# Kernel optimization log

Hardware: AMD Instinct MI355X
Metric: run time of the kernel (lower is better)

## Reference

```python
import jax, jax.numpy as jnp
import numpy as np

N_HEAD = 12
N_EMBED = 768

def setup_inputs() -> dict:
    key = jax.random.key(0)
    ks = jax.random.split(key, 5)
    B, T, C = 8, 1024, N_EMBED
    s_in = 1.0 / np.sqrt(C)
    s3 = 1.0 / np.sqrt(3 * C)
    return {
        "x": jax.random.normal(ks[0], (B, T, C), dtype=jnp.float32),
        "W_qkv": jax.random.normal(ks[1], (C, 3 * C), dtype=jnp.float32) * s_in,
        "b_qkv": jnp.zeros((3 * C,), dtype=jnp.float32),
        "W_out": jax.random.normal(ks[2], (C, C), dtype=jnp.float32) * s_in,
        "b_out": jnp.zeros((C,), dtype=jnp.float32),
    }

def reference(x, W_qkv, b_qkv, W_out, b_out):
    B, T, C = x.shape
    H = N_HEAD
    d_k = C // H
    qkv = x @ W_qkv + b_qkv  # [B,T,3C]
    q, k, v = jnp.split(qkv, 3, axis=-1)
    # [B,H,T,d]
    q = q.reshape(B, T, H, d_k).transpose(0, 2, 1, 3)
    k = k.reshape(B, T, H, d_k).transpose(0, 2, 1, 3)
    v = v.reshape(B, T, H, d_k).transpose(0, 2, 1, 3)
    logits = jnp.einsum('bhqd,bhkd->bhqk', q, k) * (d_k ** -0.5)
    causal = jnp.tril(jnp.ones((T, T), dtype=bool))
    logits = jnp.where(causal, logits, -jnp.inf)
    scores = jax.nn.softmax(logits, axis=-1)
    out = jnp.einsum('bhqk,bhkd->bhqd', scores, v)
    out = out.transpose(0, 2, 1, 3).reshape(B, T, C)
    return out @ W_out + b_out
```

## Files before the change

### kernel.cpp

```cpp
#include <hip/hip_runtime.h>
#include <stdint.h>

#define B_ 8
#define T_ 1024
#define C_ 768
#define H_ 12
#define DK 64
#define BT (B_*T_)
#define NQKV (3*C_)

typedef unsigned short u16;
typedef __bf16 bf16x8 __attribute__((ext_vector_type(8)));
typedef __bf16 bf16x4 __attribute__((ext_vector_type(4)));
typedef float  f32x4  __attribute__((ext_vector_type(4)));

typedef const __attribute__((address_space(1))) void gvoid_t;
typedef __attribute__((address_space(3))) void lvoid_t;

#define SBARRIER()  asm volatile("s_barrier" ::: "memory")
#define SWAITCNT(s) asm volatile("s_waitcnt " s ::: "memory")

__device__ __forceinline__ void gl_lds16(const void* g, void* l) {
    __builtin_amdgcn_global_load_lds((gvoid_t*)g, (lvoid_t*)l, 16, 0, 0);
}

__device__ __forceinline__ u16 f2b(float f) {
    union { float f; unsigned int u; } v; v.f = f;
    unsigned int u = v.u;
    return (u16)((u + 0x7fffu + ((u >> 16) & 1u)) >> 16);
}

__device__ __forceinline__ f32x4 mfma16(bf16x8 a, bf16x8 b, f32x4 c) {
    return __builtin_amdgcn_mfma_f32_16x16x32_bf16(a, b, c, 0, 0, 0);
}

__global__ __launch_bounds__(256)
void k_prep(const float* __restrict__ x, u16* __restrict__ xb,
            const float* __restrict__ wqkv, u16* __restrict__ wqkvT,
            const float* __restrict__ wout, u16* __restrict__ woutT)
{
    __shared__ u16 tile[32][34];
    const int bid = blockIdx.x;
    const int tid = threadIdx.x;
    if (bid < 6144) {
        int i = bid * 256 + tid;
        float4 f = ((const float4*)x)[i];
        uint2 o;
        o.x = (unsigned)f2b(f.x) | ((unsigned)f2b(f.y) << 16);
        o.y = (unsigned)f2b(f.z) | ((unsigned)f2b(f.w) << 16);
        ((uint2*)xb)[i] = o;
        return;
    }
    const float* w; u16* wt; int K, N, n0, k0;
    if (bid < 6144 + 1728) {
        int idx = bid - 6144;
        w = wqkv; wt = wqkvT; K = C_; N = NQKV;
        n0 = (idx % 72) * 32; k0 = (idx / 72) * 32;
    } else {
        int idx = bid - 7872;
        w = wout; wt = woutT; K = C_; N = C_;
        n0 = (idx % 24) * 32; k0 = (idx / 24) * 32;
    }
    const int tx = tid & 31, ty = tid >> 5;
    #pragma unroll
    for (int i = 0; i < 4; i++)
        tile[ty + i * 8][tx] = f2b(w[(size_t)(k0 + ty + i * 8) * N + n0 + tx]);
    __syncthreads();
    #pragma unroll
    for (int i = 0; i < 4; i++)
        wt[(size_t)(n0 + ty + i * 8) * K + k0 + tx] = tile[tx][ty + i * 8];
}

__global__ __launch_bounds__(256, 3)
void k_gemm_qkv(const u16* __restrict__ A, const u16* __restrict__ Bt,
                const float* __restrict__ bias,
                u16* __restrict__ qo, u16* __restrict__ ko, u16* __restrict__ vto)
{
    const int K = C_;
    __shared__ u16 As[3][128 * 32];
    __shared__ u16 Bs[3][128 * 32];
    const int tid  = threadIdx.x;
    const int lane = tid & 63;
    const int w    = tid >> 6;
    const int quad = lane >> 4;
    const int col  = lane & 15;

    const int id   = blockIdx.x + gridDim.x * blockIdx.y;
    const int xcd  = id & 7;
    const int slot = id >> 3;
    const int m0   = (xcd * 8 + (slot & 7)) * 128;
    const int n0   = (slot >> 3) * 128;

    const int wm   = (w >> 1) * 64;
    const int wn   = (w & 1) * 64;

    f32x4 zero4 = {0.f, 0.f, 0.f, 0.f};
    f32x4 acc[4][4];
    #pragma unroll
    for (int i = 0; i < 4; i++)
        #pragma unroll
        for (int j = 0; j < 4; j++) acc[i][j] = zero4;

    const int sr  = tid >> 2;
    const int scc = ((tid & 3) ^ ((sr >> 1) & 3)) * 8;
    const u16* gA = A  + (size_t)(m0 + sr) * K + scc;
    const u16* gB = Bt + (size_t)(n0 + sr) * K + scc;

    const int NIT = K >> 5;

    #define STAGE(kt, bufi)                                                          \
        do {                                                                         \
            gl_lds16(gA + (kt),                  (char*)As[bufi] + w * 1024);        \
            gl_lds16(gA + (size_t)64 * K + (kt), (char*)As[bufi] + 4096 + w * 1024); \
            gl_lds16(gB + (kt),                  (char*)Bs[bufi] + w * 1024);        \
            gl_lds16(gB + (size_t)64 * K + (kt), (char*)Bs[bufi] + 4096 + w * 1024); \
        } while (0)

    STAGE(0, 0);
    STAGE(32, 1);
    int cur = 0;
    for (int it = 0; it < NIT; ++it) {
        SBARRIER();
        if (it + 2 < NIT) {
            int b2 = cur + 2; if (b2 >= 3) b2 -= 3;
            STAGE((it + 2) << 5, b2);
            SWAITCNT("vmcnt(8)");
        } else if (it + 1 < NIT) {
            SWAITCNT("vmcnt(4)");
        } else {
            SWAITCNT("vmcnt(0)");
        }
        SBARRIER();

        const u16* Ab = As[cur];
        const u16* Bb = Bs[cur];
        bf16x8 af[4], bfr[4];
        #pragma unroll
        for (int mt = 0; mt < 4; mt++) {
            int row = wm + mt * 16 + col;
            af[mt] = *(const bf16x8*)&Ab[row * 32 + ((quad ^ ((row >> 1) & 3)) * 8)];
        }
        #pragma unroll
        for (int nt = 0; nt < 4; nt++) {
            int row = wn + nt * 16 + col;
            bfr[nt] = *(const bf16x8*)&Bb[row * 32 + ((quad ^ ((row >> 1) & 3)) * 8)];
        }
        #pragma unroll
        for (int mt = 0; mt < 4; mt++)
            #pragma unroll
            for (int nt = 0; nt < 4; nt++)
                acc[mt][nt] = mfma16(af[mt], bfr[nt], acc[mt][nt]);

        cur = (cur == 2) ? 0 : cur + 1;
    }
    #undef STAGE

    #pragma unroll
    for (int mt = 0; mt < 4; mt++) {
        #pragma unroll
        for (int nt = 0; nt < 4; nt++) {
            #pragma unroll
            for (int r = 0; r < 4; r++) {
                int m = m0 + wm + mt * 16 + quad * 4 + r;
                int n = n0 + wn + nt * 16 + col;
                float v = acc[mt][nt][r] + bias[n];
                int sec = n / C_;
                int c   = n - sec * C_;
                int h   = c >> 6;
                int d   = c & 63;
                int b   = m >> 10;
                int t   = m & 1023;
                int bh  = b * H_ + h;
                u16 bv  = f2b(v);
                if (sec == 0)      qo [((size_t)bh * T_ + t) * DK + d] = bv;
                else if (sec == 1) ko [((size_t)bh * T_ + t) * DK + d] = bv;
                else               vto[((size_t)bh * DK + d) * T_ + t] = bv;
            }
        }
    }
}

__global__ __launch_bounds__(256, 4)
void k_gemm_out(const u16* __restrict__ A, const u16* __restrict__ Bt,
                const float* __restrict__ bias, float* __restrict__ outf)
{
    const int K = C_, N = C_;
    __shared__ u16 As[3][128 * 32];
    __shared__ u16 Bs[3][64 * 32];
    const int tid  = threadIdx.x;
    const int lane = tid & 63;
    const int w    = tid >> 6;
    const int quad = lane >> 4;
    const int col  = lane & 15;

    const int id   = blockIdx.x;
    const int xcd  = id & 7;
    const int slot = id >> 3;
    const int m0   = (xcd * 8 + (slot & 7)) * 128;
    const int n0   = (slot >> 3) * 64;

    f32x4 zero4 = {0.f, 0.f, 0.f, 0.f};
    f32x4 acc[2][4];
    #pragma unroll
    for (int i = 0; i < 2; i++)
        #pragma unroll
        for (int j = 0; j < 4; j++) acc[i][j] = zero4;

    const int sr  = tid >> 2;
    const int scc = ((tid & 3) ^ ((sr >> 1) & 3)) * 8;
    const u16* gA = A  + (size_t)(m0 + sr) * K + scc;
    const u16* gB = Bt + (size_t)(n0 + sr) * K + scc;

    const int NIT = K >> 5;

    #define STAGE(kt, bufi)                                                          \
        do {                                                                         \
            gl_lds16(gA + (kt),                  (char*)As[bufi] + w * 1024);        \
            gl_lds16(gA + (size_t)64 * K + (kt), (char*)As[bufi] + 4096 + w * 1024); \
            gl_lds16(gB + (kt),                  (char*)Bs[bufi] + w * 1024);        \
        } while (0)

    STAGE(0, 0);
    STAGE(32, 1);
    int cur = 0;
    for (int it = 0; it < NIT; ++it) {
        SBARRIER();
        if (it + 2 < NIT) {
            int b2 = cur + 2; if (b2 >= 3) b2 -= 3;
            STAGE((it + 2) << 5, b2);
            SWAITCNT("vmcnt(6)");
        } else if (it + 1 < NIT) {
            SWAITCNT("vmcnt(3)");
        } else {
            SWAITCNT("vmcnt(0)");
        }
        SBARRIER();

        const u16* Ab = As[cur];
        const u16* Bb = Bs[cur];
        bf16x8 af[2], bfr[4];
        #pragma unroll
        for (int mt = 0; mt < 2; mt++) {
            int row = w * 32 + mt * 16 + col;
            af[mt] = *(const bf16x8*)&Ab[row * 32 + ((quad ^ ((row >> 1) & 3)) * 8)];
        }
        #pragma unroll
        for (int nt = 0; nt < 4; nt++) {
            int row = nt * 16 + col;
            bfr[nt] = *(const bf16x8*)&Bb[row * 32 + ((quad ^ ((row >> 1) & 3)) * 8)];
        }
        #pragma unroll
        for (int mt = 0; mt < 2; mt++)
            #pragma unroll
            for (int nt = 0; nt < 4; nt++)
                acc[mt][nt] = mfma16(af[mt], bfr[nt], acc[mt][nt]);

        cur = (cur == 2) ? 0 : cur + 1;
    }
    #undef STAGE

    #pragma unroll
    for (int mt = 0; mt < 2; mt++) {
        #pragma unroll
        for (int nt = 0; nt < 4; nt++) {
            #pragma unroll
            for (int r = 0; r < 4; r++) {
                int m = m0 + w * 32 + mt * 16 + quad * 4 + r;
                int n = n0 + nt * 16 + col;
                outf[(size_t)m * N + n] = acc[mt][nt][r] + bias[n];
            }
        }
    }
}

#define PSTRIDE 72

__device__ __forceinline__ bf16x8 ld_sw(const u16* base, int row, int half,
                                        int quad, int c7) {
    return *(const bf16x8*)(base + row * DK + (((half * 4 + quad) ^ c7) * 8));
}

template <bool MASK>
__device__ __forceinline__ void attn_chunk(
    const u16* Ks, const u16* Vs, __bf16* pbuf,
    const bf16x8 (&qf)[2][2], bf16x8 ones,
    int kv0, int qw, int quad, int col,
    f32x4 (&oacc)[2][4], f32x4 (&lacc)[2])
{
    const int c7 = col & 7;
    f32x4 zero4 = {0.f, 0.f, 0.f, 0.f};
    f32x4 st[2][4];
    #pragma unroll
    for (int g = 0; g < 4; g++) {
        bf16x8 klo = ld_sw(Ks, g * 16 + col, 0, quad, c7);
        bf16x8 khi = ld_sw(Ks, g * 16 + col, 1, quad, c7);
        st[0][g] = mfma16(khi, qf[0][1], mfma16(klo, qf[0][0], zero4));
        st[1][g] = mfma16(khi, qf[1][1], mfma16(klo, qf[1][0], zero4));
    }
    const float scl = 0.18033688f;
    #pragma unroll
    for (int s = 0; s < 2; s++) {
        __bf16* pb = pbuf + s * 16 * PSTRIDE + col * PSTRIDE;
        #pragma unroll
        for (int g = 0; g < 4; g++) {
            bf16x4 pp;
            #pragma unroll
            for (int r = 0; r < 4; r++) {
                float p = __builtin_amdgcn_exp2f(st[s][g][r] * scl - 12.0f);
                if (MASK) {
                    int kv = kv0 + g * 16 + quad * 4 + r;
                    if (kv > qw + s * 16 + col) p = 0.f;
                }
                pp[r] = (__bf16)p;
            }
            *(bf16x4*)(pb + g * 16 + quad * 4) = pp;
        }
    }
    SWAITCNT("lgkmcnt(0)");
    bf16x8 pf[2][2];
    #pragma unroll
    for (int s = 0; s < 2; s++) {
        const __bf16* pb = pbuf + s * 16 * PSTRIDE + col * PSTRIDE;
        pf[s][0] = *(const bf16x8*)(pb + quad * 8);
        pf[s][1] = *(const bf16x8*)(pb + 32 + quad * 8);
        lacc[s] = mfma16(pf[s][1], ones, mfma16(pf[s][0], ones, lacc[s]));
    }
    #pragma unroll
    for (int dt = 0; dt < 4; dt++) {
        bf16x8 vlo = ld_sw(Vs, dt * 16 + col, 0, quad, c7);
        bf16x8 vhi = ld_sw(Vs, dt * 16 + col, 1, quad, c7);
        #pragma unroll
        for (int s = 0; s < 2; s++)
            oacc[s][dt] = mfma16(pf[s][1], vhi, mfma16(pf[s][0], vlo, oacc[s][dt]));
    }
}

__global__ __launch_bounds__(256, 3)
void k_attn(const u16* __restrict__ Q, const u16* __restrict__ Kf,
            const u16* __restrict__ Vt, u16* __restrict__ Of)
{
    __shared__ u16 Ks[2][64 * DK];
    __shared__ u16 Vs[2][64 * DK];
    __shared__ __bf16 Plds[4][32 * PSTRIDE];
    const int bh   = blockIdx.x;
    const int b    = bh / H_;
    const int h    = bh - b * H_;
    const int tid  = threadIdx.x;
    const int lane = tid & 63;
    const int w    = tid >> 6;
    const int quad = lane >> 4;
    const int col  = lane & 15;
    const int ty   = 7 - (int)blockIdx.y;
    const int nch  = 2 * ty + 2;
    const int qw   = ty * 128 + w * 32;
    __bf16* pbuf = Plds[w];

    const u16* Qb = Q  + (size_t)bh * T_ * DK;
    const u16* Kb = Kf + (size_t)bh * T_ * DK;
    const u16* Vb = Vt + (size_t)bh * DK * T_;

    int sG0 = tid, sG1 = 256 + tid;
    int sr0 = sG0 >> 3, sg0 = (sG0 & 7) ^ (sr0 & 7);
    int sr1 = sG1 >> 3, sg1 = (sG1 & 7) ^ (sr1 & 7);

    bf16x8 qf[2][2];
    #pragma unroll
    for (int s = 0; s < 2; s++) {
        const u16* qp = Qb + (size_t)(qw + s * 16 + col) * DK;
        qf[s][0] = *(const bf16x8*)(qp + quad * 8);
        qf[s][1] = *(const bf16x8*)(qp + 32 + quad * 8);
    }

    bf16x8 ones;
    #pragma unroll
    for (int i = 0; i < 8; i++) ((u16*)&ones)[i] = 0x3F80;

    f32x4 zero4 = {0.f, 0.f, 0.f, 0.f};
    f32x4 oacc[2][4];
    f32x4 lacc[2] = {zero4, zero4};
    #pragma unroll
    for (int s = 0; s < 2; s++)
        #pragma unroll
        for (int dt = 0; dt < 4; dt++) oacc[s][dt] = zero4;

    #define ASTAGE(c, bufi)                                                            \
        do {                                                                           \
            int kvs = (c) * 64;                                                        \
            gl_lds16(Kb + (size_t)(kvs + sr0) * DK + sg0 * 8, (char*)Ks[bufi] + w * 1024);        \
            gl_lds16(Kb + (size_t)(kvs + sr1) * DK + sg1 * 8, (char*)Ks[bufi] + 4096 + w * 1024); \
            gl_lds16(Vb + (size_t)sr0 * T_ + kvs + sg0 * 8,   (char*)Vs[bufi] + w * 1024);        \
            gl_lds16(Vb + (size_t)sr1 * T_ + kvs + sg1 * 8,   (char*)Vs[bufi] + 4096 + w * 1024); \
        } while (0)

    ASTAGE(0, 0);
    #pragma unroll 1
    for (int c = 0; c < nch; ++c) {
        const int cur = c & 1;
        SBARRIER();
        if (c + 1 < nch) {
            ASTAGE(c + 1, cur ^ 1);
            SWAITCNT("vmcnt(4)");
        } else {
            SWAITCNT("vmcnt(0)");
        }
        SBARRIER();

        const int kv0 = c * 64;
        if (kv0 <= qw + 31) {
            if (kv0 + 63 <= qw)
                attn_chunk<false>(Ks[cur], Vs[cur], pbuf, qf, ones, kv0, qw, quad, col, oacc, lacc);
            else
                attn_chunk<true>(Ks[cur], Vs[cur], pbuf, qf, ones, kv0, qw, quad, col, oacc, lacc);
        }
    }
    #undef ASTAGE

    #pragma unroll
    for (int s = 0; s < 2; s++) {
        #pragma unroll
        for (int r = 0; r < 4; r++) {
            float inv = 1.f / lacc[s][r];
            int t = qw + s * 16 + quad * 4 + r;
            u16* op = Of + ((size_t)(b * T_ + t)) * C_ + h * DK;
            #pragma unroll
            for (int dt = 0; dt < 4; dt++) op[dt * 16 + col] = f2b(oacc[s][dt][r] * inv);
        }
    }
}

extern "C" void kernel_launch(void* const* d_in, const int* in_sizes, int n_in,
                              void* d_out, int out_size, void* d_ws, size_t ws_size,
                              hipStream_t stream) {
    const float* x    = (const float*)d_in[0];
    const float* Wqkv = (const float*)d_in[1];
    const float* bqkv = (const float*)d_in[2];
    const float* Wout = (const float*)d_in[3];
    const float* bout = (const float*)d_in[4];
    float* out = (float*)d_out;

    char* ws = (char*)d_ws;
    u16* xb    = (u16*)(ws);
    u16* wqkvT = (u16*)(ws + 12582912);
    u16* woutT = (u16*)(ws + 16121856);
    u16* qw    = (u16*)(ws + 17301504);
    u16* kw    = (u16*)(ws + 29884416);
    u16* vtw   = (u16*)(ws + 42467328);
    u16* aw    = (u16*)(ws + 55050240);

    k_prep<<<8448, 256, 0, stream>>>(x, xb, Wqkv, wqkvT, Wout, woutT);

    k_gemm_qkv<<<dim3(NQKV / 128, BT / 128), 256, 0, stream>>>(
        xb, wqkvT, bqkv, qw, kw, vtw);

    k_attn<<<dim3(B_ * H_, 8), 256, 0, stream>>>(qw, kw, vtw, aw);

    k_gemm_out<<<768, 256, 0, stream>>>(aw, woutT, bout, out);
}
```

Measured before the change: 183.0 us.

## Enlarge QKV GEMM to 256x256 tiles with 8 waves and interleaved prefetch

Rewrites the QKV projection GEMM to use 512-thread blocks that each compute a 256x256 output tile with a 64-wide K step. Global-to-LDS loads are split into quarter stages interleaved with MFMA quadrants, with s_setprio raised around the MFMA bursts. The launch becomes 288 blocks mapped per XCD. The aim is more operand reuse per LDS byte and better overlap of loads with matrix math, at the cost of fewer, larger blocks (possible wave-quantization on the CU count), higher register pressure, and many more barriers.

New measurement: 209.3 us. +14.4%, slower.

```diff
diff --git a/kernel.cpp b/kernel.cpp
--- a/kernel.cpp
+++ b/kernel.cpp
@@ -71,110 +71,156 @@
         wt[(size_t)(n0 + ty + i * 8) * K + k0 + tx] = tile[tx][ty + i * 8];
 }
 
-__global__ __launch_bounds__(256, 3)
+__global__ __launch_bounds__(512, 2)
 void k_gemm_qkv(const u16* __restrict__ A, const u16* __restrict__ Bt,
                 const float* __restrict__ bias,
                 u16* __restrict__ qo, u16* __restrict__ ko, u16* __restrict__ vto)
 {
     const int K = C_;
-    __shared__ u16 As[3][128 * 32];
-    __shared__ u16 Bs[3][128 * 32];
+    __shared__ u16 As[2][2][256 * 32];
+    __shared__ u16 Bs[2][2][256 * 32];
+
     const int tid  = threadIdx.x;
     const int lane = tid & 63;
     const int w    = tid >> 6;
     const int quad = lane >> 4;
     const int col  = lane & 15;
-
-    const int id   = blockIdx.x + gridDim.x * blockIdx.y;
+    const int wm2  = w >> 2;
+    const int wn4  = w & 3;
+
+    const int id   = blockIdx.x;
     const int xcd  = id & 7;
-    const int slot = id >> 3;
-    const int m0   = (xcd * 8 + (slot & 7)) * 128;
-    const int n0   = (slot >> 3) * 128;
-
-    const int wm   = (w >> 1) * 64;
-    const int wn   = (w & 1) * 64;
+    const int s    = id >> 3;
+    const int sm   = s / 9;
+    const int m0   = (xcd * 4 + sm) * 256;
+    const int n0   = (s - sm * 9) * 256;
 
     f32x4 zero4 = {0.f, 0.f, 0.f, 0.f};
-    f32x4 acc[4][4];
-    #pragma unroll
-    for (int i = 0; i < 4; i++)
+    f32x4 acc[8][4];
+    #pragma unroll
+    for (int i = 0; i < 8; i++)
         #pragma unroll
         for (int j = 0; j < 4; j++) acc[i][j] = zero4;
+    bf16x8 af[4][2], bf[4][2];
 
     const int sr  = tid >> 2;
     const int scc = ((tid & 3) ^ ((sr >> 1) & 3)) * 8;
     const u16* gA = A  + (size_t)(m0 + sr) * K + scc;
     const u16* gB = Bt + (size_t)(n0 + sr) * K + scc;
 
-    const int NIT = K >> 5;
-
-    #define STAGE(kt, bufi)                                                          \
-        do {                                                                         \
-            gl_lds16(gA + (kt),                  (char*)As[bufi] + w * 1024);        \
-            gl_lds16(gA + (size_t)64 * K + (kt), (char*)As[bufi] + 4096 + w * 1024); \
-            gl_lds16(gB + (kt),                  (char*)Bs[bufi] + w * 1024);        \
-            gl_lds16(gB + (size_t)64 * K + (kt), (char*)Bs[bufi] + 4096 + w * 1024); \
+    const int arow  = wm2 * 128 + col;
+    const int a_off = arow * 32 + ((quad ^ ((arow >> 1) & 3)) * 8);
+    const int brow  = wn4 * 64 + col;
+    const int b_off = brow * 32 + ((quad ^ ((brow >> 1) & 3)) * 8);
+
+    const int NIT = K >> 6;
+
+    #define SU(unit, gsrc, koff)                                                      \
+        do {                                                                          \
+            gl_lds16((gsrc) + (koff),                   (char*)(unit) + w * 1024);    \
+            gl_lds16((gsrc) + (size_t)128 * K + (koff), (char*)(unit) + 8192 + w * 1024); \
         } while (0)
 
-    STAGE(0, 0);
-    STAGE(32, 1);
-    int cur = 0;
-    for (int it = 0; it < NIT; ++it) {
-        SBARRIER();
-        if (it + 2 < NIT) {
-            int b2 = cur + 2; if (b2 >= 3) b2 -= 3;
-            STAGE((it + 2) << 5, b2);
-            SWAITCNT("vmcnt(8)");
-        } else if (it + 1 < NIT) {
-            SWAITCNT("vmcnt(4)");
-        } else {
-            SWAITCNT("vmcnt(0)");
-        }
-        SBARRIER();
-
-        const u16* Ab = As[cur];
-        const u16* Bb = Bs[cur];
-        bf16x8 af[4], bfr[4];
-        #pragma unroll
-        for (int mt = 0; mt < 4; mt++) {
-            int row = wm + mt * 16 + col;
-            af[mt] = *(const bf16x8*)&Ab[row * 32 + ((quad ^ ((row >> 1) & 3)) * 8)];
-        }
-        #pragma unroll
-        for (int nt = 0; nt < 4; nt++) {
-            int row = wn + nt * 16 + col;
-            bfr[nt] = *(const bf16x8*)&Bb[row * 32 + ((quad ^ ((row >> 1) & 3)) * 8)];
-        }
-        #pragma unroll
-        for (int mt = 0; mt < 4; mt++)
-            #pragma unroll
-            for (int nt = 0; nt < 4; nt++)
-                acc[mt][nt] = mfma16(af[mt], bfr[nt], acc[mt][nt]);
-
-        cur = (cur == 2) ? 0 : cur + 1;
-    }
-    #undef STAGE
-
-    #pragma unroll
-    for (int mt = 0; mt < 4; mt++) {
-        #pragma unroll
-        for (int nt = 0; nt < 4; nt++) {
+    #define MFMA_Q(MB, NB)                                                            \
+        __builtin_amdgcn_s_setprio(1);                                                \
+        _Pragma("unroll")                                                             \
+        for (int mf = 0; mf < 4; mf++)                                                \
+            _Pragma("unroll")                                                         \
+            for (int nf = 0; nf < 2; nf++)                                            \
+                acc[(MB) + mf][(NB) + nf] = mfma16(af[mf][1], bf[(NB) + nf][1],       \
+                    mfma16(af[mf][0], bf[(NB) + nf][0], acc[(MB) + mf][(NB) + nf]));  \
+        __builtin_amdgcn_s_setprio(0)
+
+    #define KTILE(T, D)                                                               \
+        do {                                                                          \
+            const u16* Ac0 = As[D][0]; const u16* Ac1 = As[D][1];                     \
+            const u16* Bc0 = Bs[D][0]; const u16* Bc1 = Bs[D][1];                     \
+            const bool pA = (T) + 1 < NIT;                                            \
+            const bool pB = (T) + 2 < NIT;                                            \
+            const int  kA = ((T) + 1) << 6;                                           \
+            const int  kB = ((T) + 2) << 6;                                           \
+                        \
+            _Pragma("unroll")                                                         \
+            for (int mf = 0; mf < 4; mf++) {                                          \
+                af[mf][0] = *(const bf16x8*)&Ac0[a_off + mf * 512];                   \
+                af[mf][1] = *(const bf16x8*)&Ac1[a_off + mf * 512];                   \
+            }                                                                         \
+            _Pragma("unroll")                                                         \
+            for (int nf = 0; nf < 2; nf++) {                                          \
+                bf[nf][0] = *(const bf16x8*)&Bc0[b_off + nf * 512];                   \
+                bf[nf][1] = *(const bf16x8*)&Bc1[b_off + nf * 512];                   \
+            }                                                                         \
+            if (pA) SU(As[(D) ^ 1][0], gA, kA);                                       \
+            SBARRIER();                                                               \
+            MFMA_Q(0, 0);                                                             \
+            SBARRIER();                                                               \
+                                   \
+            _Pragma("unroll")                                                         \
+            for (int nf = 2; nf < 4; nf++) {                                          \
+                bf[nf][0] = *(const bf16x8*)&Bc0[b_off + nf * 512];                   \
+                bf[nf][1] = *(const bf16x8*)&Bc1[b_off + nf * 512];                   \
+            }                                                                         \
+            if (pA) SU(As[(D) ^ 1][1], gA, kA + 32);                                  \
+            SBARRIER();                                                               \
+            MFMA_Q(0, 2);                                                             \
+            SBARRIER();                                                               \
+                    \
+            _Pragma("unroll")                                                         \
+            for (int mf = 0; mf < 4; mf++) {                                          \
+                af[mf][0] = *(const bf16x8*)&Ac0[a_off + (mf + 4) * 512];             \
+                af[mf][1] = *(const bf16x8*)&Ac1[a_off + (mf + 4) * 512];             \
+            }                                                                         \
+            if (pB) SU(Bs[D][0], gB, kB);                                             \
+            SBARRIER();                                                               \
+            MFMA_Q(4, 0);                                                             \
+            SBARRIER();                                                               \
+                     \
+            if (pB) SU(Bs[D][1], gB, kB + 32);                                        \
+            if (pB) { SWAITCNT("vmcnt(4)"); } else { SWAITCNT("vmcnt(0)"); }          \
+            SBARRIER();                                                               \
+            MFMA_Q(4, 2);                                                             \
+            SBARRIER();                                                               \
+        } while (0)
+
+    SU(As[0][0], gA, 0);
+    SU(As[0][1], gA, 32);
+    SU(Bs[0][0], gB, 0);
+    SU(Bs[0][1], gB, 32);
+    SU(Bs[1][0], gB, 64);
+    SU(Bs[1][1], gB, 96);
+    SWAITCNT("vmcnt(4)");
+    SBARRIER();
+
+    #pragma unroll 1
+    for (int tt = 0; tt < NIT / 2; ++tt) {
+        KTILE(2 * tt, 0);
+        KTILE(2 * tt + 1, 1);
+    }
+    #undef KTILE
+    #undef MFMA_Q
+    #undef SU
+
+    #pragma unroll
+    for (int nf = 0; nf < 4; nf++) {
+        const int nbase = n0 + wn4 * 64 + nf * 16;
+        const int sec   = nbase / C_;
+        const int cbase = nbase - sec * C_;
+        const int h     = cbase >> 6;
+        const int dd    = (cbase & 63) + col;
+        const float bn  = bias[nbase + col];
+        #pragma unroll
+        for (int mf = 0; mf < 8; mf++) {
+            const int mrow = m0 + wm2 * 128 + mf * 16 + quad * 4;
+            const int b    = mrow >> 10;
+            const int t0   = mrow & 1023;
+            const int bh   = b * H_ + h;
             #pragma unroll
             for (int r = 0; r < 4; r++) {
-                int m = m0 + wm + mt * 16 + quad * 4 + r;
-                int n = n0 + wn + nt * 16 + col;
-                float v = acc[mt][nt][r] + bias[n];
-                int sec = n / C_;
-                int c   = n - sec * C_;
-                int h   = c >> 6;
-                int d   = c & 63;
-                int b   = m >> 10;
-                int t   = m & 1023;
-                int bh  = b * H_ + h;
-                u16 bv  = f2b(v);
-                if (sec == 0)      qo [((size_t)bh * T_ + t) * DK + d] = bv;
-                else if (sec == 1) ko [((size_t)bh * T_ + t) * DK + d] = bv;
-                else               vto[((size_t)bh * DK + d) * T_ + t] = bv;
+                u16 bv = f2b(acc[mf][nf][r] + bn);
+                const int t = t0 + r;
+                if (sec == 0)      qo [((size_t)bh * T_ + t) * DK + dd] = bv;
+                else if (sec == 1) ko [((size_t)bh * T_ + t) * DK + dd] = bv;
+                else               vto[((size_t)bh * DK + dd) * T_ + t] = bv;
             }
         }
     }
@@ -449,8 +495,7 @@
 
     k_prep<<<8448, 256, 0, stream>>>(x, xb, Wqkv, wqkvT, Wout, woutT);
 
-    k_gemm_qkv<<<dim3(NQKV / 128, BT / 128), 256, 0, stream>>>(
-        xb, wqkvT, bqkv, qw, kw, vtw);
+    k_gemm_qkv<<<288, 512, 0, stream>>>(xb, wqkvT, bqkv, qw, kw, vtw);
 
     k_attn<<<dim3(B_ * H_, 8), 256, 0, stream>>>(qw, kw, vtw, aw);
 
```
